# Kernel tuning notes

Measured on AMD Instinct MI355X. Metric: run time of the kernel, lower is better.

Reference implementation:

```python
import jax, jax.numpy as jnp
import numpy as np

NX, NY = 512, 512
DX, DY = 1e-4, 1e-4
VS = 1550.0
DT = 2.5e-8


def setup_inputs() -> dict:
    key = jax.random.key(0)
    k1, k2 = jax.random.split(key)
    sensor_data = jax.random.normal(k1, (4, 2, 128, 2048), dtype=jnp.float32)
    sensor_xy = jax.random.randint(k2, (128, 2), 0, 512, dtype=jnp.int32)
    return {"sensor_data": sensor_data, "sensor_xy": sensor_xy}


def _delay_indices(sensor_xy):
    # pixel grids, 1-indexed as in the torch code (arange(1,513))
    ix = jnp.arange(1, NX + 1, dtype=jnp.float32)[None, :, None]  # (1,Nx,1)
    iy = jnp.arange(1, NY + 1, dtype=jnp.float32)[None, None, :]  # (1,1,Ny)
    x = sensor_xy[:, 0].astype(jnp.float32)[:, None, None]        # (S,1,1)
    y = sensor_xy[:, 1].astype(jnp.float32)[:, None, None]
    dis = jnp.sqrt(((x - ix + 1.0) * DX) ** 2 + ((y - iy + 1.0) * DY) ** 2)  # (S,Nx,Ny)
    # .to(torch.long) truncates; values are non-negative so int cast matches
    return (dis / VS / DT).astype(jnp.int32).reshape(sensor_xy.shape[0], -1)  # (S, Nx*Ny)


def reference(sensor_data, sensor_xy):
    B = sensor_data.shape[0]
    S = sensor_xy.shape[0]
    t = _delay_indices(sensor_xy)                           # (S, P) int32
    data = jnp.transpose(sensor_data, (2, 0, 1, 3))         # (S, B, 2, T)

    def step(img, xs):
        t_s, d_s = xs                                       # (P,), (B,2,T)
        return img + d_s[:, :, t_s], None                   # gather + accumulate

    img0 = jnp.zeros((B, 2, NX * NY), dtype=sensor_data.dtype)
    img, _ = jax.lax.scan(step, img0, (t, data))
    return img.reshape(B, 2, NX, NY)
```

## Files before the change

### kernel.cpp

```cpp
#include <hip/hip_runtime.h>
#include <math.h>


#define NXY 512
#define S_CNT 128
#define T_CNT 2048
#define CH 8
#define CH_STRIDE (S_CNT * T_CNT)
#define NPIX (NXY * NXY)
#define TAB_BYTES (NPIX * 2)

#pragma float_control(push)
#pragma float_control(precise, on)
__device__ __forceinline__ unsigned short delay_entry(int adx, int ady) {
    const double DX32 = (double)1e-4f;
    const double R1 = (double)(float)(1.0 / 1550.0);
    const double R2 = (double)(float)(1.0 / (double)2.5e-8f);
    float dxf = (float)((double)adx * DX32);
    float dyf = (float)((double)ady * DX32);
    float a2 = (float)((double)dxf * (double)dxf);
    float b2 = (float)((double)dyf * (double)dyf);
    float sum = (float)((double)a2 + (double)b2);
    float dis = (float)sqrt((double)sum);
    float q1 = (float)((double)dis * R1);
    float q2 = (float)((double)q1 * R2);
    return (unsigned short)(int)q2;
}

__device__ __forceinline__ unsigned int bf16_rne(float f) {
    unsigned int x = __float_as_uint(f);
    return (x + 0x7fffu + ((x >> 16) & 1u)) >> 16;
}

__global__ __launch_bounds__(256) void prep(const float* __restrict__ data,
                                            unsigned short* __restrict__ tab,
                                            uint4* __restrict__ d2b) {
    int idx = blockIdx.x * 256 + threadIdx.x;
    tab[idx] = delay_entry(idx >> 9, idx & 511);

    unsigned int w[4];
#pragma unroll
    for (int j = 0; j < 4; ++j) {
        unsigned int lo = bf16_rne(data[(2 * j) * CH_STRIDE + idx]);
        unsigned int hi = bf16_rne(data[(2 * j + 1) * CH_STRIDE + idx]);
        w[j] = lo | (hi << 16);
    }
    d2b[idx] = make_uint4(w[0], w[1], w[2], w[3]);
}
#pragma float_control(pop)

__device__ __forceinline__ float bflo(unsigned int u) { return __uint_as_float(u << 16); }
__device__ __forceinline__ float bfhi(unsigned int u) { return __uint_as_float(u & 0xffff0000u); }

__global__ __launch_bounds__(256) void das_gather8b(const uint4* __restrict__ d2b,
                                                    const unsigned short* __restrict__ tab,
                                                    const int* __restrict__ sxy,
                                                    float* __restrict__ out) {
    __shared__ int sx[S_CNT];
    __shared__ int sy[S_CNT];
    int tid = threadIdx.x;
    if (tid < S_CNT) {
        sx[tid] = sxy[2 * tid];
        sy[tid] = sxy[2 * tid + 1];
    }
    __syncthreads();

    int iy = ((blockIdx.x & 31) << 4) | (((tid >> 6) & 1) << 3) | (tid & 7);
    int ix = ((blockIdx.x >> 5) << 4) | ((tid >> 7) << 3) | ((tid >> 3) & 7);

    float acc[CH];
#pragma unroll
    for (int k = 0; k < CH; ++k) acc[k] = 0.0f;

#pragma unroll 4
    for (int s = 0; s < S_CNT; ++s) {
        int dxi = sx[s] - ix;
        int dyi = sy[s] - iy;
        int adx = dxi < 0 ? -dxi : dxi;
        int ady = dyi < 0 ? -dyi : dyi;
        int t = (int)tab[(adx << 9) | ady];
        uint4 w = d2b[(s << 11) + t];
        acc[0] += bflo(w.x);
        acc[1] += bfhi(w.x);
        acc[2] += bflo(w.y);
        acc[3] += bfhi(w.y);
        acc[4] += bflo(w.z);
        acc[5] += bfhi(w.z);
        acc[6] += bflo(w.w);
        acc[7] += bfhi(w.w);
    }

    int pix = (ix << 9) | iy;
#pragma unroll
    for (int k = 0; k < CH; ++k) out[k * NPIX + pix] = acc[k];
}

#pragma float_control(push)
#pragma float_control(precise, on)
__global__ __launch_bounds__(256) void build_table(unsigned short* __restrict__ tab) {
    int idx = blockIdx.x * 256 + threadIdx.x;
    tab[idx] = delay_entry(idx >> 9, idx & 511);
}
#pragma float_control(pop)

__global__ __launch_bounds__(256) void das_main(const float* __restrict__ data,
                                                const unsigned short* __restrict__ tab,
                                                const int* __restrict__ sxy,
                                                float* __restrict__ out) {
    __shared__ int sx[S_CNT];
    __shared__ int sy[S_CNT];
    int tid = threadIdx.x;
    if (tid < S_CNT) {
        sx[tid] = sxy[2 * tid];
        sy[tid] = sxy[2 * tid + 1];
    }
    __syncthreads();
    int iy = ((blockIdx.x & 31) << 4) | (tid & 15);
    int ix = ((blockIdx.x >> 5) << 4) | (tid >> 4);
    float acc[CH];
#pragma unroll
    for (int k = 0; k < CH; ++k) acc[k] = 0.0f;
#pragma unroll 4
    for (int s = 0; s < S_CNT; ++s) {
        int dxi = sx[s] - ix;
        int dyi = sy[s] - iy;
        int adx = dxi < 0 ? -dxi : dxi;
        int ady = dyi < 0 ? -dyi : dyi;
        int t = (int)tab[(adx << 9) | ady];
        const float* p = data + (s << 11) + t;
#pragma unroll
        for (int k = 0; k < CH; ++k) acc[k] += p[(size_t)k * CH_STRIDE];
    }
    int pix = (ix << 9) | iy;
#pragma unroll
    for (int k = 0; k < CH; ++k) out[k * NPIX + pix] = acc[k];
}

extern "C" void kernel_launch(void* const* d_in, const int* in_sizes, int n_in,
                              void* d_out, int out_size, void* d_ws, size_t ws_size,
                              hipStream_t stream) {
    const float* data = (const float*)d_in[0];
    const int* sxy = (const int*)d_in[1];
    float* out = (float*)d_out;
    unsigned short* tab = (unsigned short*)d_ws;

    size_t need = (size_t)TAB_BYTES + (size_t)CH_STRIDE * 16;
    if (ws_size >= need) {
        uint4* d2b = (uint4*)((char*)d_ws + TAB_BYTES);
        prep<<<NPIX / 256, 256, 0, stream>>>(data, tab, d2b);
        das_gather8b<<<1024, 256, 0, stream>>>(d2b, tab, sxy, out);
    } else {
        build_table<<<NPIX / 256, 256, 0, stream>>>(tab);
        das_main<<<1024, 256, 0, stream>>>(data, tab, sxy, out);
    }
}
```

Before: 96.46 us.

## Stage per-tile delay windows and table patches in LDS for gather

Each 16x16 pixel tile now computes, per sensor, the minimum distance and delay to the tile. In chunks of 32 sensors it stages a 64-entry window of packed bf16 samples and a 16x24 patch of the delay table into shared memory. The inner loop then reads delay and sample data from LDS instead of issuing scattered global gathers. This adds cooperative loads, barriers and about 60KB of LDS per block, which may lower occupancy. It also assumes the delay spread across a tile fits in 64 samples and the patch in 24 columns.

```diff
diff --git a/kernel.cpp b/kernel.cpp
--- a/kernel.cpp
+++ b/kernel.cpp
@@ -9,6 +9,10 @@
 #define CH_STRIDE (S_CNT * T_CNT)
 #define NPIX (NXY * NXY)
 #define TAB_BYTES (NPIX * 2)
+#define CHUNK 32
+#define NCHUNK (S_CNT / CHUNK)
+#define WIN 64
+#define PATW 24
 
 #pragma float_control(push)
 #pragma float_control(precise, on)
@@ -47,47 +51,96 @@
     }
     d2b[idx] = make_uint4(w[0], w[1], w[2], w[3]);
 }
+
+__device__ __forceinline__ int tmin_entry(int adx, int ady) {
+    return (int)delay_entry(adx, ady);
+}
 #pragma float_control(pop)
 
 __device__ __forceinline__ float bflo(unsigned int u) { return __uint_as_float(u << 16); }
 __device__ __forceinline__ float bfhi(unsigned int u) { return __uint_as_float(u & 0xffff0000u); }
 
-__global__ __launch_bounds__(256) void das_gather8b(const uint4* __restrict__ d2b,
-                                                    const unsigned short* __restrict__ tab,
-                                                    const int* __restrict__ sxy,
-                                                    float* __restrict__ out) {
-    __shared__ int sx[S_CNT];
-    __shared__ int sy[S_CNT];
+__global__ __launch_bounds__(256) void das_gather_lds(const uint4* __restrict__ d2b,
+                                                      const unsigned short* __restrict__ tab,
+                                                      const int* __restrict__ sxy,
+                                                      float* __restrict__ out) {
+    __shared__ int4 meta[S_CNT];
+    __shared__ uint4 winb[CHUNK * WIN];
+    __shared__ uint4 patb[CHUNK * 16 * 3];
+    const unsigned short* pat16 = (const unsigned short*)patb;
+
     int tid = threadIdx.x;
+    int x0 = (blockIdx.x >> 5) << 4;
+    int y0 = (blockIdx.x & 31) << 4;
+
     if (tid < S_CNT) {
-        sx[tid] = sxy[2 * tid];
-        sy[tid] = sxy[2 * tid + 1];
+        int sxv = sxy[2 * tid];
+        int syv = sxy[2 * tid + 1];
+        int axm = sxv < x0 ? x0 - sxv : (sxv > x0 + 15 ? sxv - x0 - 15 : 0);
+        int aym = syv < y0 ? y0 - syv : (syv > y0 + 15 ? syv - y0 - 15 : 0);
+        int ay0 = aym & ~7;
+        int tmin = tmin_entry(axm, aym);
+        meta[tid] = make_int4(sxv, syv, axm | (ay0 << 16), tmin);
     }
     __syncthreads();
 
-    int iy = ((blockIdx.x & 31) << 4) | (((tid >> 6) & 1) << 3) | (tid & 7);
-    int ix = ((blockIdx.x >> 5) << 4) | ((tid >> 7) << 3) | ((tid >> 3) & 7);
+    int iy = y0 | (((tid >> 6) & 1) << 3) | (tid & 7);
+    int ix = x0 | ((tid >> 7) << 3) | ((tid >> 3) & 7);
 
     float acc[CH];
 #pragma unroll
     for (int k = 0; k < CH; ++k) acc[k] = 0.0f;
 
+    for (int c = 0; c < NCHUNK; ++c) {
+        int s0 = c * CHUNK;
+
+        {
+            int lsw = tid >> 3;
+            int tm = meta[s0 + lsw].w;
+            const uint4* src = d2b + ((s0 + lsw) << 11) + tm;
+            int e0 = tid & 7;
+#pragma unroll
+            for (int j = 0; j < 8; ++j)
+                winb[(lsw << 6) + e0 + 8 * j] = src[e0 + 8 * j];
+        }
+
+#pragma unroll
+        for (int j = 0; j < 6; ++j) {
+            unsigned int idx = (unsigned int)tid + 256u * j;
+            unsigned int r3 = idx / 3u;
+            unsigned int cc = idx - r3 * 3u;
+            unsigned int row = r3 & 15u;
+            unsigned int ls = r3 >> 4;
+            int4 m = meta[s0 + ls];
+            int ax0 = m.z & 0xffff;
+            int ay0 = m.z >> 16;
+            const uint4* src = (const uint4*)((const char*)tab +
+                (((size_t)(ax0 + (int)row) << 10) + ((size_t)ay0 << 1) + ((size_t)cc << 4)));
+            patb[ls * 48u + row * 3u + cc] = *src;
+        }
+        __syncthreads();
+
 #pragma unroll 4
-    for (int s = 0; s < S_CNT; ++s) {
-        int dxi = sx[s] - ix;
-        int dyi = sy[s] - iy;
-        int adx = dxi < 0 ? -dxi : dxi;
-        int ady = dyi < 0 ? -dyi : dyi;
-        int t = (int)tab[(adx << 9) | ady];
-        uint4 w = d2b[(s << 11) + t];
-        acc[0] += bflo(w.x);
-        acc[1] += bfhi(w.x);
-        acc[2] += bflo(w.y);
-        acc[3] += bfhi(w.y);
-        acc[4] += bflo(w.z);
-        acc[5] += bfhi(w.z);
-        acc[6] += bflo(w.w);
-        acc[7] += bfhi(w.w);
+        for (int ls = 0; ls < CHUNK; ++ls) {
+            int4 m = meta[s0 + ls];
+            int dxi = m.x - ix;
+            int dyi = m.y - iy;
+            int adx = dxi < 0 ? -dxi : dxi;
+            int ady = dyi < 0 ? -dyi : dyi;
+            int ax0 = m.z & 0xffff;
+            int ay0 = m.z >> 16;
+            int t = (int)pat16[ls * (16 * PATW) + (adx - ax0) * PATW + (ady - ay0)];
+            uint4 w = winb[(ls << 6) + (t - m.w)];
+            acc[0] += bflo(w.x);
+            acc[1] += bfhi(w.x);
+            acc[2] += bflo(w.y);
+            acc[3] += bfhi(w.y);
+            acc[4] += bflo(w.z);
+            acc[5] += bfhi(w.z);
+            acc[6] += bflo(w.w);
+            acc[7] += bfhi(w.w);
+        }
+        __syncthreads();
     }
 
     int pix = (ix << 9) | iy;
@@ -148,7 +201,7 @@
     if (ws_size >= need) {
         uint4* d2b = (uint4*)((char*)d_ws + TAB_BYTES);
         prep<<<NPIX / 256, 256, 0, stream>>>(data, tab, d2b);
-        das_gather8b<<<1024, 256, 0, stream>>>(d2b, tab, sxy, out);
+        das_gather_lds<<<1024, 256, 0, stream>>>(d2b, tab, sxy, out);
     } else {
         build_table<<<NPIX / 256, 256, 0, stream>>>(tab);
         das_main<<<1024, 256, 0, stream>>>(data, tab, sxy, out);
```

Result: slower. 106.0 us (+9.8%).
